# Optimization experiments

Measured on AMD Instinct MI355X. Metric: run time of the kernel, lower is better.

The kernel has to match this reference:

```python
import jax, jax.numpy as jnp
import numpy as np

B, S, SR, SN = 8, 1024, 256, 1024
D1 = 768; D2 = 512; D3 = 768; MVH = 256
H = 12; HDC = 32; HDR = 32; HD = 64
MLP_DIM = 3072
LN_EPS = 1e-6

def _ln(x, w):
    mu = jnp.mean(x, axis=-1, keepdims=True)
    var = jnp.var(x, axis=-1, keepdims=True)
    return (x - mu) * jax.lax.rsqrt(var + LN_EPS) * w

def _rope(x, freqs):
    # x: [B,H,S,dr]; freqs: [S, dr//2] (learned RoPE param)
    emb = jnp.concatenate([freqs, freqs], axis=-1)
    cos = jnp.cos(emb); sin = jnp.sin(emb)
    d = x.shape[-1] // 2
    rot = jnp.concatenate([-x[..., d:], x[..., :d]], axis=-1)
    return x * cos + rot * sin

def _rope_freqs(seq, dim, theta=10.0):
    inv_freq = 1.0 / theta ** (np.arange(0, dim, 2, dtype=np.float32) / dim)
    t = np.arange(seq, dtype=np.float32)
    return jnp.asarray(np.outer(t, inv_freq))

def setup_inputs():
    key = jax.random.key(0)
    ks = iter(jax.random.split(key, 48))
    n = lambda shape, s=0.02: jax.random.normal(next(ks), shape, jnp.float32) * s
    return dict(
        input_q=jax.random.normal(next(ks), (B, S, D1), jnp.float32),
        ln_q_w=jnp.ones((D1,), jnp.float32), ln_kv_w=jnp.ones((D1,), jnp.float32),
        Wt_mq=n((SR, S)), Wt_vq=n((SR, S)), Wt_mkv=n((SR, S)), Wt_vkv=n((SR, S)),
        mq_w1=n((D2, D1)), mq_w2=n((MVH, D2)),
        vq_w1=n((D2, D1)), vq_w2=n((MVH, D2)),
        mkv_w1=n((D2, D1)), mkv_w2=n((MVH, D2)),
        vkv_w1=n((D2, D1)), vkv_w2=n((MVH, D2)),
        dirty_zq=n((1, SR, MVH), 1.0), dirty_zkv=n((1, SR, MVH), 1.0),
        e2de=jnp.array([1.0], jnp.float32),
        Wt_qzu=n((SN, SR)), Wt_kzu=n((SN, SR)), Wt_vzu=n((SN, SR)),
        Wt_qr=n((SN, SR)), Wt_kr=n((SN, S)),
        qz_up=n((D2, MVH)), kz_up=n((D2, MVH)), vz_up=n((D2, MVH)),
        q_w=n((H * HDC, D2)), k_w=n((H * HDC, D2)), v_w=n((D3, D2)),
        qr_w=n((H * HDR, MVH)), kr_w=n((H * HDR, D1)),
        rope_q_freqs=_rope_freqs(SN, HDR), rope_k_freqs=_rope_freqs(SN, HDR),
        out_w=n((D3, D3)), ln2_w=jnp.ones((D3,), jnp.float32),
        mlp_w1=n((MLP_DIM, D3)), mlp_w2=n((D3, MLP_DIM)),
        eps_zq=jax.random.normal(next(ks), (B, SR, MVH), jnp.float32),
        eps_zkv=jax.random.normal(next(ks), (B, SR, MVH), jnp.float32),
    )

def reference(input_q, ln_q_w, ln_kv_w, Wt_mq, Wt_vq, Wt_mkv, Wt_vkv, mq_w1, mq_w2, vq_w1, vq_w2, mkv_w1, mkv_w2, vkv_w1, vkv_w2, dirty_zq, dirty_zkv, e2de, Wt_qzu, Wt_kzu, Wt_vzu, Wt_qr, Wt_kr, qz_up, kz_up, vz_up, q_w, k_w, v_w, qr_w, kr_w, rope_q_freqs, rope_k_freqs, out_w, ln2_w, mlp_w1, mlp_w2, eps_zq, eps_zkv):
    lin = lambda x, w: x @ w.T                       # torch Linear: W is [out, in]
    tlin = lambda x, w: jnp.einsum('bsd,rs->brd', x, w)  # Linear along seq axis
    xq = _ln(input_q, ln_q_w)
    xkv = _ln(input_q, ln_kv_w)  # input_kv = input_q (self-attention)
    # latent VAE mean/var: seq compress S->SR then feature D1->D2->MVH
    mean_zq = lin(lin(tlin(xq, Wt_mq), mq_w1), mq_w2)
    var_zq = lin(lin(tlin(xq, Wt_vq), vq_w1), vq_w2)
    mean_zkv = lin(lin(tlin(xkv, Wt_mkv), mkv_w1), mkv_w2)
    var_zkv = lin(lin(tlin(xkv, Wt_vkv), vkv_w1), vkv_w2)
    zq = mean_zq + (e2de * eps_zq + (1.0 - e2de) * dirty_zq) * jnp.exp(0.5 * var_zq)
    zkv = mean_zkv + (e2de * eps_zkv + (1.0 - e2de) * dirty_zkv) * jnp.exp(0.5 * var_zkv)
    # upsample seq SR->SN and features MVH->D2
    qz = lin(tlin(zq, Wt_qzu), qz_up)
    kz = lin(tlin(zkv, Wt_kzu), kz_up)
    vz = lin(tlin(zkv, Wt_vzu), vz_up)
    qr = lin(tlin(zq, Wt_qr), qr_w)        # [B,SN,H*HDR]
    kr = lin(tlin(input_q, Wt_kr), kr_w)   # [B,SN,H*HDR]
    qz = lin(qz, q_w); kz = lin(kz, k_w); vz = lin(vz, v_w)
    heads = lambda t, d: t.reshape(B, SN, H, d).transpose(0, 2, 1, 3)
    q = jnp.concatenate([heads(qz, HDC), _rope(heads(qr, HDR), rope_q_freqs)], axis=-1)
    k = jnp.concatenate([heads(kz, HDC), _rope(heads(kr, HDR), rope_k_freqs)], axis=-1)
    v = heads(vz, HD)
    scores = jnp.einsum('bhqd,bhkd->bhqk', q, k) / jnp.sqrt(jnp.float32(HD))
    o = jnp.einsum('bhqk,bhkd->bhqd', jax.nn.softmax(scores, axis=-1), v)
    o = o.transpose(0, 2, 1, 3).reshape(B, SN, D3)
    x = lin(o, out_w) + input_q
    y = _ln(x, ln2_w)
    y = lin(jax.nn.gelu(lin(y, mlp_w1), approximate=False), mlp_w2)
    return x + y
```

## Files before the change

kernel.cpp:

```cpp
#include <hip/hip_runtime.h>
#include <math.h>

#define B_   8
#define S_   1024
#define SR_  256
#define SN_  1024
#define D1_  768
#define D2_  512
#define D3_  768
#define MVH_ 256
#define H_   12
#define HD_  64
#define MLP_ 3072

typedef __attribute__((ext_vector_type(8))) short bf16x8;
typedef __attribute__((ext_vector_type(4))) float f32x4;

__device__ inline ushort f2bf(float f) {
  uint u = __float_as_uint(f);
  uint r = (u + 0x7fffu + ((u >> 16) & 1u)) >> 16;
  return (ushort)r;
}
__device__ inline float b2f(ushort u) { return __uint_as_float(((uint)u) << 16); }

__device__ inline void gload16(const void* g, void* l) {
  __builtin_amdgcn_global_load_lds(
      (const __attribute__((address_space(1))) void*)g,
      (__attribute__((address_space(3))) void*)l, 16, 0, 0);
}

__device__ inline int xcd_swz(int lin, int n) {
  int xcd = lin & 7, idx = lin >> 3;
  int q = n >> 3, r = n & 7;
  return (xcd < r ? xcd * (q + 1) : r * (q + 1) + (xcd - r) * q) + idx;
}

__global__ __launch_bounds__(256) void ln_dual_b(const float* __restrict__ x,
    const float* __restrict__ w1, const float* __restrict__ w2,
    ushort* __restrict__ o1, ushort* __restrict__ o2, int D) {
  int row = blockIdx.x;
  const float* xr = x + (size_t)row * D;
  int tid = threadIdx.x;
  float s = 0.f, ss = 0.f;
  for (int i = tid; i < D; i += 256) { float v = xr[i]; s += v; ss += v * v; }
  __shared__ float rs[256];
  __shared__ float rq[256];
  rs[tid] = s; rq[tid] = ss;
  __syncthreads();
  for (int off = 128; off > 0; off >>= 1) {
    if (tid < off) { rs[tid] += rs[tid + off]; rq[tid] += rq[tid + off]; }
    __syncthreads();
  }
  float mu  = rs[0] / (float)D;
  float var = rq[0] / (float)D - mu * mu;
  float inv = rsqrtf(var + 1e-6f);
  for (int i = tid; i < D; i += 256) {
    float v = (xr[i] - mu) * inv;
    o1[(size_t)row * D + i] = f2bf(v * w1[i]);
    o2[(size_t)row * D + i] = f2bf(v * w2[i]);
  }
}

__global__ __launch_bounds__(256) void ln_b(const float* __restrict__ x,
    const float* __restrict__ w, ushort* __restrict__ o, int D) {
  int row = blockIdx.x;
  const float* xr = x + (size_t)row * D;
  int tid = threadIdx.x;
  float s = 0.f, ss = 0.f;
  for (int i = tid; i < D; i += 256) { float v = xr[i]; s += v; ss += v * v; }
  __shared__ float rs[256];
  __shared__ float rq[256];
  rs[tid] = s; rq[tid] = ss;
  __syncthreads();
  for (int off = 128; off > 0; off >>= 1) {
    if (tid < off) { rs[tid] += rs[tid + off]; rq[tid] += rq[tid + off]; }
    __syncthreads();
  }
  float mu  = rs[0] / (float)D;
  float var = rq[0] / (float)D - mu * mu;
  float inv = rsqrtf(var + 1e-6f);
  for (int i = tid; i < D; i += 256) {
    float v = (xr[i] - mu) * inv;
    o[(size_t)row * D + i] = f2bf(v * w[i]);
  }
}

__global__ __launch_bounds__(256) void trans_f2b(const float* __restrict__ in,
    ushort* __restrict__ out, int R, int C, long strideEl) {
  __shared__ float tile[32][33];
  int bb = blockIdx.z;
  const float* ib = in + (size_t)bb * strideEl;
  ushort* ob = out + (size_t)bb * strideEl;
  int c0 = blockIdx.x << 5, r0 = blockIdx.y << 5;
  int tx = threadIdx.x & 31, ty = threadIdx.x >> 5;
#pragma unroll
  for (int i = 0; i < 4; ++i)
    tile[ty + 8 * i][tx] = ib[(size_t)(r0 + ty + 8 * i) * C + c0 + tx];
  __syncthreads();
#pragma unroll
  for (int i = 0; i < 4; ++i)
    ob[(size_t)(c0 + ty + 8 * i) * R + r0 + tx] = f2bf(tile[tx][ty + 8 * i]);
}

__global__ __launch_bounds__(256) void trans_b2b(const ushort* __restrict__ in,
    ushort* __restrict__ out, int R, int C, long strideEl) {
  __shared__ ushort tile[32][33];
  int bb = blockIdx.z;
  const ushort* ib = in + (size_t)bb * strideEl;
  ushort* ob = out + (size_t)bb * strideEl;
  int c0 = blockIdx.x << 5, r0 = blockIdx.y << 5;
  int tx = threadIdx.x & 31, ty = threadIdx.x >> 5;
#pragma unroll
  for (int i = 0; i < 4; ++i)
    tile[ty + 8 * i][tx] = ib[(size_t)(r0 + ty + 8 * i) * C + c0 + tx];
  __syncthreads();
#pragma unroll
  for (int i = 0; i < 4; ++i)
    ob[(size_t)(c0 + ty + 8 * i) * R + r0 + tx] = tile[tx][ty + 8 * i];
}

struct ConvTab {
  const float* src[28];
  int off[28];
  int cum[29];
};
__global__ __launch_bounds__(256) void multi_f2b(ConvTab t, ushort* __restrict__ wb,
                                                 int total4) {
  int i = blockIdx.x * 256 + threadIdx.x;
  if (i >= total4) return;
  int ti = 0;
  while (t.cum[ti + 1] <= i) ++ti;
  int j = i - t.cum[ti];
  float4 v = ((const float4*)t.src[ti])[j];
  ushort4 o;
  o.x = f2bf(v.x); o.y = f2bf(v.y); o.z = f2bf(v.z); o.w = f2bf(v.w);
  ((ushort4*)(wb + t.off[ti]))[j] = o;
}

__global__ __launch_bounds__(256) void rope_tab(const float* __restrict__ fq,
    const float* __restrict__ fk, float* __restrict__ ctq, float* __restrict__ stq,
    float* __restrict__ ctk, float* __restrict__ stk, int n) {
  int i = blockIdx.x * 256 + threadIdx.x;
  if (i >= n) return;
  float a = fq[i]; ctq[i] = cosf(a); stq[i] = sinf(a);
  float c = fk[i]; ctk[i] = cosf(c); stk[i] = sinf(c);
}

template <int EPI>
__global__ __launch_bounds__(256) void gemm_bf16(const ushort* __restrict__ A, long sA,
    const ushort* __restrict__ Bm, long sB, const float* __restrict__ R,
    void* __restrict__ Cout, long sC, int M, int N, int K) {
  int gx = gridDim.x, gy = gridDim.y;
  int nwg = gx * gy * gridDim.z;
  int lin = ((int)blockIdx.z * gy + (int)blockIdx.y) * gx + (int)blockIdx.x;
  lin = xcd_swz(lin, nwg);
  int bx = lin % gx, tt = lin / gx;
  int by = tt % gy, bb = tt / gy;
  const ushort* Ab = A + (size_t)bb * sA;
  const ushort* Bb = Bm + (size_t)bb * sB;
  __shared__ ushort As[128 * 32];
  __shared__ ushort Bs[128 * 32];
  int tid = threadIdx.x;
  int lane = tid & 63, wid = tid >> 6;
  int m0 = by << 7, n0 = bx << 7;
  int wm = (wid >> 1) << 6, wn = (wid & 1) << 6;
  f32x4 acc[4][4];
#pragma unroll
  for (int i = 0; i < 4; ++i)
#pragma unroll
    for (int j = 0; j < 4; ++j) acc[i][j] = (f32x4){0.f, 0.f, 0.f, 0.f};
  char* asb = (char*)As;
  char* bsb = (char*)Bs;
  int srow = lane >> 2;
  int skb  = (lane & 3) << 4;
  for (int k0 = 0; k0 < K; k0 += 32) {
    __syncthreads();
#pragma unroll
    for (int i = 0; i < 2; ++i) {
      int rr = wid * 32 + i * 16;
      gload16((const char*)Ab + ((size_t)(m0 + rr + srow) * K + k0) * 2 + skb,
              asb + rr * 64);
      gload16((const char*)Bb + ((size_t)(n0 + rr + srow) * K + k0) * 2 + skb,
              bsb + rr * 64);
    }
    __syncthreads();
    bf16x8 af[4], bf[4];
#pragma unroll
    for (int m = 0; m < 4; ++m)
      af[m] = *(bf16x8*)&As[(wm + m * 16 + (lane & 15)) * 32 + ((lane >> 4) << 3)];
#pragma unroll
    for (int n = 0; n < 4; ++n)
      bf[n] = *(bf16x8*)&Bs[(wn + n * 16 + (lane & 15)) * 32 + ((lane >> 4) << 3)];
#pragma unroll
    for (int m = 0; m < 4; ++m)
#pragma unroll
      for (int n = 0; n < 4; ++n)
        acc[m][n] = __builtin_amdgcn_mfma_f32_16x16x32_bf16(af[m], bf[n], acc[m][n], 0, 0, 0);
  }
  int cr = (lane >> 4) << 2, cc = lane & 15;
#pragma unroll
  for (int m = 0; m < 4; ++m)
#pragma unroll
    for (int n = 0; n < 4; ++n) {
#pragma unroll
      for (int r = 0; r < 4; ++r) {
        int row = m0 + wm + m * 16 + cr + r;
        int col = n0 + wn + n * 16 + cc;
        float v = acc[m][n][r];
        if (EPI == 0) {
          ((ushort*)Cout)[(size_t)bb * sC + (size_t)row * N + col] = f2bf(v);
        } else if (EPI == 1) {
          ((float*)Cout)[(size_t)row * N + col] = v + R[(size_t)row * N + col];
        } else {
          float y = 0.7978845608f * (v + 0.044715f * v * v * v);
          float sg = 1.0f / (1.0f + __expf(-2.0f * y));
          ((ushort*)Cout)[(size_t)row * N + col] = f2bf(v * sg);
        }
      }
    }
}

struct GrpTab {
  const ushort* A[32];
  const ushort* Bm[32];
  ushort* C[32];
};
__global__ __launch_bounds__(256) void gemm_grp(GrpTab t, int M, int N, int K) {
  int gx = gridDim.x, gy = gridDim.y;
  int nwg = gx * gy * gridDim.z;
  int lin = ((int)blockIdx.z * gy + (int)blockIdx.y) * gx + (int)blockIdx.x;
  lin = xcd_swz(lin, nwg);
  int bx = lin % gx, tt = lin / gx;
  int by = tt % gy, zz = tt / gy;
  const ushort* Ab = t.A[zz];
  const ushort* Bb = t.Bm[zz];
  ushort* Cb = t.C[zz];
  __shared__ ushort As[128 * 32];
  __shared__ ushort Bs[128 * 32];
  int tid = threadIdx.x;
  int lane = tid & 63, wid = tid >> 6;
  int m0 = by << 7, n0 = bx << 7;
  int wm = (wid >> 1) << 6, wn = (wid & 1) << 6;
  f32x4 acc[4][4];
#pragma unroll
  for (int i = 0; i < 4; ++i)
#pragma unroll
    for (int j = 0; j < 4; ++j) acc[i][j] = (f32x4){0.f, 0.f, 0.f, 0.f};
  char* asb = (char*)As;
  char* bsb = (char*)Bs;
  int srow = lane >> 2;
  int skb  = (lane & 3) << 4;
  for (int k0 = 0; k0 < K; k0 += 32) {
    __syncthreads();
#pragma unroll
    for (int i = 0; i < 2; ++i) {
      int rr = wid * 32 + i * 16;
      gload16((const char*)Ab + ((size_t)(m0 + rr + srow) * K + k0) * 2 + skb,
              asb + rr * 64);
      gload16((const char*)Bb + ((size_t)(n0 + rr + srow) * K + k0) * 2 + skb,
              bsb + rr * 64);
    }
    __syncthreads();
    bf16x8 af[4], bf[4];
#pragma unroll
    for (int m = 0; m < 4; ++m)
      af[m] = *(bf16x8*)&As[(wm + m * 16 + (lane & 15)) * 32 + ((lane >> 4) << 3)];
#pragma unroll
    for (int n = 0; n < 4; ++n)
      bf[n] = *(bf16x8*)&Bs[(wn + n * 16 + (lane & 15)) * 32 + ((lane >> 4) << 3)];
#pragma unroll
    for (int m = 0; m < 4; ++m)
#pragma unroll
      for (int n = 0; n < 4; ++n)
        acc[m][n] = __builtin_amdgcn_mfma_f32_16x16x32_bf16(af[m], bf[n], acc[m][n], 0, 0, 0);
  }
  int cr = (lane >> 4) << 2, cc = lane & 15;
#pragma unroll
  for (int m = 0; m < 4; ++m)
#pragma unroll
    for (int n = 0; n < 4; ++n) {
#pragma unroll
      for (int r = 0; r < 4; ++r) {
        int row = m0 + wm + m * 16 + cr + r;
        int col = n0 + wn + n * 16 + cc;
        Cb[(size_t)row * N + col] = f2bf(acc[m][n][r]);
      }
    }
}

__global__ __launch_bounds__(256) void z_combine_b(const ushort* __restrict__ mean,
    const ushort* __restrict__ var, const float* __restrict__ eps,
    const float* __restrict__ dirty, const float* __restrict__ e2de_p,
    ushort* __restrict__ zout, int total, int perBatch) {
  int i = blockIdx.x * 256 + threadIdx.x;
  if (i >= total) return;
  float e = e2de_p[0];
  float v = b2f(mean[i]) +
            (e * eps[i] + (1.0f - e) * dirty[i % perBatch]) * expf(0.5f * b2f(var[i]));
  zout[i] = f2bf(v);
}

__global__ __launch_bounds__(256) void pack_qk_b8(const ushort* __restrict__ zf,
    const ushort* __restrict__ rf, const float* __restrict__ ct,
    const float* __restrict__ st, ushort* __restrict__ out, float scale) {
  int i8 = blockIdx.x * 256 + threadIdx.x;
  int i = i8 << 3;
  int d0 = i & 63;
  int s = (i >> 6) & (S_ - 1);
  int bh = i >> 16;
  int b = bh / H_, h = bh % H_;
  short res[8];
  if (d0 < 32) {
    bf16x8 v = *(const bf16x8*)(zf + ((size_t)(b * S_ + s)) * (H_ * 32) + h * 32 + d0);
#pragma unroll
    for (int j = 0; j < 8; ++j) res[j] = (short)f2bf(b2f((ushort)v[j]) * scale);
  } else {
    const ushort* xr = rf + ((size_t)(b * S_ + s)) * (H_ * 32) + h * 32;
    int dr0 = d0 - 32;
    if (dr0 < 16) {
      bf16x8 xa = *(const bf16x8*)(xr + dr0);
      bf16x8 xb2 = *(const bf16x8*)(xr + dr0 + 16);
#pragma unroll
      for (int j = 0; j < 8; ++j) {
        float c = ct[s * 16 + dr0 + j], sn = st[s * 16 + dr0 + j];
        res[j] = (short)f2bf((b2f((ushort)xa[j]) * c - b2f((ushort)xb2[j]) * sn) * scale);
      }
    } else {
      bf16x8 xa = *(const bf16x8*)(xr + dr0);
      bf16x8 xb2 = *(const bf16x8*)(xr + dr0 - 16);
#pragma unroll
      for (int j = 0; j < 8; ++j) {
        float c = ct[s * 16 + dr0 - 16 + j], sn = st[s * 16 + dr0 - 16 + j];
        res[j] = (short)f2bf((b2f((ushort)xa[j]) * c + b2f((ushort)xb2[j]) * sn) * scale);
      }
    }
  }
  *(bf16x8*)(out + i) = *(bf16x8*)res;
}

__global__ __launch_bounds__(256) void pack_v_b8(const ushort* __restrict__ vzf,
    ushort* __restrict__ out) {
  int i8 = blockIdx.x * 256 + threadIdx.x;
  int i = i8 << 3;
  int d0 = i & 63;
  int s = (i >> 6) & (S_ - 1);
  int bh = i >> 16;
  int b = bh / H_, h = bh % H_;
  bf16x8 v = *(const bf16x8*)(vzf + ((size_t)(b * S_ + s)) * D3_ + h * 64 + d0);
  *(bf16x8*)(out + i) = v;
}

__global__ __launch_bounds__(256) void attn_mfma(const ushort* __restrict__ Q,
    const ushort* __restrict__ K, const ushort* __restrict__ V,
    ushort* __restrict__ O) {
  __shared__ ushort lds[16384];
  char* qc = (char*)lds;
  char* kc = (char*)lds + 8192;
  char* vc = (char*)lds + 16384;
  char* pc = (char*)lds + 24576;
  int tid = threadIdx.x, lane = tid & 63, wid = tid >> 6;
  int nwg = gridDim.x * gridDim.y;
  int lin = (int)blockIdx.y * gridDim.x + (int)blockIdx.x;
  lin = xcd_swz(lin, nwg);
  int qt = lin % gridDim.x;
  int bh = lin / gridDim.x;
  int q0 = qt << 6;
  int b = bh / H_, h = bh % H_;
  const ushort* Qb = Q + ((size_t)bh * S_ + q0) * HD_;
  const ushort* Kb = K + (size_t)bh * S_ * HD_;
  const ushort* Vb = V + (size_t)bh * S_ * HD_;
  {
    int r = tid >> 2, c0 = (tid & 3) * 32;
    const char* src = (const char*)Qb + r * 128;
    uint4 v0 = *(const uint4*)(src + c0);
    uint4 v1 = *(const uint4*)(src + c0 + 16);
    int sw = (r & 7) << 4;
    *(uint4*)(qc + r * 128 + (c0 ^ sw)) = v0;
    *(uint4*)(qc + r * 128 + ((c0 + 16) ^ sw)) = v1;
  }
  __syncthreads();
  bf16x8 aq[2];
  {
    int r = wid * 16 + (lane & 15);
    int sw = (r & 7) << 4;
#pragma unroll
    for (int kk = 0; kk < 2; ++kk) {
      int c2 = kk * 64 + ((lane >> 4) << 4);
      aq[kk] = *(bf16x8*)(qc + r * 128 + (c2 ^ sw));
    }
  }
  f32x4 o_[4];
  float m_[4], l_[4];
#pragma unroll
  for (int i = 0; i < 4; ++i) { o_[i] = (f32x4){0.f,0.f,0.f,0.f}; m_[i] = -1e30f; l_[i] = 0.f; }

  for (int kt = 0; kt < S_ / 64; ++kt) {
    __syncthreads();
    {
      int r = tid >> 2, c0 = (tid & 3) * 32;
      const char* src = (const char*)(Kb + (size_t)(kt * 64 + r) * HD_);
      uint4 v0 = *(const uint4*)(src + c0);
      uint4 v1 = *(const uint4*)(src + c0 + 16);
      int sw = (r & 7) << 4;
      *(uint4*)(kc + r * 128 + (c0 ^ sw)) = v0;
      *(uint4*)(kc + r * 128 + ((c0 + 16) ^ sw)) = v1;
    }
    {
      int kp = tid & 31, g = tid >> 5, d0 = g * 8;
      const ushort* s0 = Vb + (size_t)(kt * 64 + 2 * kp) * HD_ + d0;
      bf16x8 va = *(const bf16x8*)s0;
      bf16x8 vb2 = *(const bf16x8*)(s0 + HD_);
#pragma unroll
      for (int j = 0; j < 8; ++j) {
        int d = d0 + j;
        uint val = (uint)(ushort)va[j] | ((uint)(ushort)vb2[j] << 16);
        *(uint*)(vc + d * 128 + ((kp * 4) ^ ((d & 7) << 4))) = val;
      }
    }
    __syncthreads();
    f32x4 sacc[4];
#pragma unroll
    for (int ksub = 0; ksub < 4; ++ksub) {
      sacc[ksub] = (f32x4){0.f,0.f,0.f,0.f};
#pragma unroll
      for (int kk = 0; kk < 2; ++kk) {
        int r = ksub * 16 + (lane & 15);
        int c2 = kk * 64 + ((lane >> 4) << 4);
        bf16x8 bk = *(bf16x8*)(kc + r * 128 + (c2 ^ ((r & 7) << 4)));
        sacc[ksub] = __builtin_amdgcn_mfma_f32_16x16x32_bf16(aq[kk], bk, sacc[ksub], 0, 0, 0);
      }
    }
    float p[4][4];
#pragma unroll
    for (int rr = 0; rr < 4; ++rr) {
      float cm = fmaxf(fmaxf(sacc[0][rr], sacc[1][rr]), fmaxf(sacc[2][rr], sacc[3][rr]));
      cm = fmaxf(cm, __shfl_xor(cm, 1));
      cm = fmaxf(cm, __shfl_xor(cm, 2));
      cm = fmaxf(cm, __shfl_xor(cm, 4));
      cm = fmaxf(cm, __shfl_xor(cm, 8));
      float mn = fmaxf(m_[rr], cm);
      float al = __expf(m_[rr] - mn);
      float ps = 0.f;
#pragma unroll
      for (int ksub = 0; ksub < 4; ++ksub) {
        float pv = __expf(sacc[ksub][rr] - mn);
        p[ksub][rr] = pv;
        ps += pv;
      }
      ps += __shfl_xor(ps, 1);
      ps += __shfl_xor(ps, 2);
      ps += __shfl_xor(ps, 4);
      ps += __shfl_xor(ps, 8);
      l_[rr] = l_[rr] * al + ps;
      m_[rr] = mn;
#pragma unroll
      for (int ds = 0; ds < 4; ++ds) o_[ds][rr] *= al;
    }
#pragma unroll
    for (int ksub = 0; ksub < 4; ++ksub)
#pragma unroll
      for (int rr = 0; rr < 4; ++rr) {
        int r = wid * 16 + ((lane >> 4) << 2) + rr;
        int cb = (ksub * 16 + (lane & 15)) * 2;
        *(ushort*)(pc + r * 128 + (cb ^ ((r & 7) << 4))) = f2bf(p[ksub][rr]);
      }
#pragma unroll
    for (int kk2 = 0; kk2 < 2; ++kk2) {
      int rA = wid * 16 + (lane & 15);
      int c2 = kk2 * 64 + ((lane >> 4) << 4);
      bf16x8 ap = *(bf16x8*)(pc + rA * 128 + (c2 ^ ((rA & 7) << 4)));
#pragma unroll
      for (int ds = 0; ds < 4; ++ds) {
        int rB = ds * 16 + (lane & 15);
        bf16x8 bv = *(bf16x8*)(vc + rB * 128 + (c2 ^ ((rB & 7) << 4)));
        o_[ds] = __builtin_amdgcn_mfma_f32_16x16x32_bf16(ap, bv, o_[ds], 0, 0, 0);
      }
    }
  }
#pragma unroll
  for (int rr = 0; rr < 4; ++rr) {
    float inv = 1.f / l_[rr];
    int q = q0 + wid * 16 + ((lane >> 4) << 2) + rr;
#pragma unroll
    for (int ds = 0; ds < 4; ++ds) {
      int d = ds * 16 + (lane & 15);
      O[((size_t)(b * S_ + q)) * D3_ + h * HD_ + d] = f2bf(o_[ds][rr] * inv);
    }
  }
}

extern "C" void kernel_launch(void* const* d_in, const int* in_sizes, int n_in,
                              void* d_out, int out_size, void* d_ws, size_t ws_size,
                              hipStream_t stream) {
  const float* input_q = (const float*)d_in[0];
  const float* ln_q_w  = (const float*)d_in[1];
  const float* ln_kv_w = (const float*)d_in[2];
  const float* dirty_zq  = (const float*)d_in[15];
  const float* dirty_zkv = (const float*)d_in[16];
  const float* e2de    = (const float*)d_in[17];
  const float* rope_q_f = (const float*)d_in[31];
  const float* rope_k_f = (const float*)d_in[32];
  const float* ln2_w   = (const float*)d_in[34];
  const float* eps_zq  = (const float*)d_in[37];
  const float* eps_zkv = (const float*)d_in[38];

  ushort* wsu = (ushort*)d_ws;
  ushort* wb    = wsu;
  ushort* xq_b  = wsu + 12124160;
  ushort* xkv_b = wsu + 18415616;
  ushort* xqT   = wsu + 37289984;
  ushort* xkvT  = wsu + 43581440;
  ushort* inT   = wsu + 49872896;
  ushort* t1q   = wsu + 12124160;
  ushort* t1kv  = wsu + 15269888;
  ushort* t2b   = wsu + 24707072;
  ushort* mv    = wsu + 28901376;
  ushort* zqb   = wsu + 30998528;
  ushort* zkvb  = wsu + 31522816;
  ushort* zqT   = wsu + 32047104;
  ushort* zkvT  = wsu + 32571392;
  ushort* up    = wsu + 12124160;
  ushort* vzf   = wsu + 20512768;
  ushort* mid   = wsu + 56164352;
  ushort* tkr   = wsu + 37289984;
  ushort* qzf   = wsu + 68747264;
  ushort* kzf   = wsu + 71892992;
  ushort* qrf   = wsu + 75038720;
  ushort* krf   = wsu + 78184448;
  float*  ctq   = (float*)(wsu + 81330176);
  float*  stq   = ctq + 16384;
  float*  ctk   = ctq + 32768;
  float*  stk   = ctq + 49152;
  ushort* qp    = wsu + 12124160;
  ushort* kp    = wsu + 43581440;
  ushort* vp    = wsu + 49872896;
  ushort* ofb   = wsu + 56164352;
  float*  xb    = (float*)(wsu + 12124160);
  ushort* ylb   = wsu + 37289984;
  ushort* hm    = wsu + 43581440;

  const int W_mq = 0,       W_mkv = 524288;
  const int Wq1 = 1048576,  Wv1 = 1441792,  Wk1 = 1835008,  Wkv1 = 2228224;
  const int Wq2 = 2621440,  Wv2 = 2752512,  Wk2 = 2883584,  Wkv2 = 3014656;
  const int W_qzu = 3145728, W_kzu = 3407872, W_vzu = 3670016, W_qr = 3932160;
  const int W_kr = 4194304, W_qzup = 5242880, W_kzup = 5373952, W_vzup = 5505024;
  const int W_qw = 5636096, W_kw = 5832704,  W_vw = 6029312,  W_qrw = 6422528;
  const int W_krw = 6520832, W_ow = 6815744, W_m1 = 7405568,  W_m2 = 9764864;

  ln_dual_b<<<B_ * S_, 256, 0, stream>>>(input_q, ln_q_w, ln_kv_w, xq_b, xkv_b, D1_);

  {
    dim3 g(D1_ / 32, S_ / 32, B_);
    trans_b2b<<<g, 256, 0, stream>>>(xq_b, xqT, S_, D1_, (long)S_ * D1_);
    trans_b2b<<<g, 256, 0, stream>>>(xkv_b, xkvT, S_, D1_, (long)S_ * D1_);
    trans_f2b<<<g, 256, 0, stream>>>(input_q, inT, S_, D1_, (long)S_ * D1_);
  }

  {
    ConvTab t;
    const int srcIdx[28] = {3,4,5,6, 7,9,11,13, 8,10,12,14, 18,19,20,21, 22,
                            23,24,25, 26,27, 28, 29, 30, 33, 35, 36};
    const int sz[28] = {262144,262144,262144,262144, 393216,393216,393216,393216,
                        131072,131072,131072,131072, 262144,262144,262144,262144,
                        1048576, 131072,131072,131072, 196608,196608, 393216,
                        98304, 294912, 589824, 2359296, 2359296};
    int off = 0, c4 = 0;
    for (int i = 0; i < 28; ++i) {
      t.src[i] = (const float*)d_in[srcIdx[i]];
      t.off[i] = off;
      t.cum[i] = c4;
      off += sz[i];
      c4 += sz[i] / 4;
    }
    t.cum[28] = c4;
    multi_f2b<<<(c4 + 255) / 256, 256, 0, stream>>>(t, wb, c4);
    rope_tab<<<64, 256, 0, stream>>>(rope_q_f, rope_k_f, ctq, stq, ctk, stk, 16384);
  }

  long sXT = (long)S_ * D1_;

  {
    GrpTab t;
    for (int c = 0; c < 2; ++c)
      for (int b = 0; b < 8; ++b) {
        int z = c * 8 + b;
        t.A[z] = wb + (c == 0 ? W_mq : W_mkv);
        t.Bm[z] = (c == 0 ? xqT : xkvT) + (size_t)b * sXT;
        t.C[z] = (c == 0 ? t1q : t1kv) + (size_t)b * 512 * 768;
      }
    dim3 g(D1_ / 128, 512 / 128, 16);
    gemm_grp<<<g, 256, 0, stream>>>(t, 512, D1_, S_);
  }
  {
    GrpTab t;
    const int wo[4] = {Wq1, Wv1, Wk1, Wkv1};
    for (int c = 0; c < 4; ++c)
      for (int b = 0; b < 8; ++b) {
        int z = c * 8 + b;
        ushort* t1 = (c < 2 ? t1q : t1kv);
        t.A[z] = t1 + (size_t)b * 512 * 768 + (size_t)(c & 1) * 256 * 768;
        t.Bm[z] = wb + wo[c];
        t.C[z] = t2b + (size_t)z * 256 * 512;
      }
    dim3 g(D2_ / 128, 256 / 128, 32);
    gemm_grp<<<g, 256, 0, stream>>>(t, 256, D2_, D1_);
  }
  {
    GrpTab t;
    const int wo[4] = {Wq2, Wv2, Wk2, Wkv2};
    for (int c = 0; c < 4; ++c)
      for (int b = 0; b < 8; ++b) {
        int z = c * 8 + b;
        t.A[z] = t2b + (size_t)z * 256 * 512;
        t.Bm[z] = wb + wo[c];
        t.C[z] = mv + (size_t)z * 256 * 256;
      }
    dim3 g(MVH_ / 128, 256 / 128, 32);
    gemm_grp<<<g, 256, 0, stream>>>(t, 256, MVH_, D2_);
  }
  z_combine_b<<<(B_ * SR_ * MVH_) / 256, 256, 0, stream>>>(mv, mv + 8 * 65536,
      eps_zq, dirty_zq, e2de, zqb, B_ * SR_ * MVH_, SR_ * MVH_);
  z_combine_b<<<(B_ * SR_ * MVH_) / 256, 256, 0, stream>>>(mv + 16 * 65536,
      mv + 24 * 65536, eps_zkv, dirty_zkv, e2de, zkvb, B_ * SR_ * MVH_, SR_ * MVH_);
  {
    dim3 g(MVH_ / 32, SR_ / 32, B_);
    trans_b2b<<<g, 256, 0, stream>>>(zqb, zqT, SR_, MVH_, (long)SR_ * MVH_);
    trans_b2b<<<g, 256, 0, stream>>>(zkvb, zkvT, SR_, MVH_, (long)SR_ * MVH_);
  }
  {
    GrpTab t;
    const int wo[4] = {W_qzu, W_kzu, W_vzu, W_qr};
    for (int c = 0; c < 4; ++c)
      for (int b = 0; b < 8; ++b) {
        int z = c * 8 + b;
        t.A[z] = wb + wo[c];
        t.Bm[z] = ((c == 0 || c == 3) ? zqT : zkvT) + (size_t)b * 65536;
        t.C[z] = up + (size_t)z * 1024 * 256;
      }
    dim3 g(MVH_ / 128, SN_ / 128, 32);
    gemm_grp<<<g, 256, 0, stream>>>(t, SN_, MVH_, SR_);
  }
  {
    GrpTab t;
    const int wo[3] = {W_qzup, W_kzup, W_vzup};
    for (int c = 0; c < 3; ++c) {
      t.A[c] = up + (size_t)c * 8 * 1024 * 256;
      t.Bm[c] = wb + wo[c];
      t.C[c] = mid + (size_t)c * 8192 * 512;
    }
    dim3 g(D2_ / 128, (B_ * SN_) / 128, 3);
    gemm_grp<<<g, 256, 0, stream>>>(t, B_ * SN_, D2_, MVH_);
  }
  {
    dim3 g(384 / 128, (B_ * SN_) / 128, 1);
    gemm_bf16<0><<<g, 256, 0, stream>>>(up + (size_t)3 * 8 * 1024 * 256, 0,
        wb + W_qrw, 0, nullptr, qrf, 0, B_ * SN_, 384, MVH_);
  }
  {
    GrpTab t;
    t.A[0] = mid;                      t.Bm[0] = wb + W_qw; t.C[0] = qzf;
    t.A[1] = mid + (size_t)8192 * 512; t.Bm[1] = wb + W_kw; t.C[1] = kzf;
    dim3 g(384 / 128, (B_ * SN_) / 128, 2);
    gemm_grp<<<g, 256, 0, stream>>>(t, B_ * SN_, 384, D2_);
  }
  {
    dim3 g(D3_ / 128, (B_ * SN_) / 128, 1);
    gemm_bf16<0><<<g, 256, 0, stream>>>(mid + (size_t)2 * 8192 * 512, 0,
        wb + W_vw, 0, nullptr, vzf, 0, B_ * SN_, D3_, D2_);
  }
  {
    dim3 g(D1_ / 128, SN_ / 128, B_);
    gemm_bf16<0><<<g, 256, 0, stream>>>(wb + W_kr, 0, inT, sXT, nullptr, tkr,
        (long)SN_ * D1_, SN_, D1_, S_);
  }
  {
    dim3 g(384 / 128, (B_ * SN_) / 128, 1);
    gemm_bf16<0><<<g, 256, 0, stream>>>(tkr, 0, wb + W_krw, 0, nullptr, krf, 0,
        B_ * SN_, 384, D1_);
  }

  int chunks = (B_ * H_ * S_ * HD_) / 8;
  pack_qk_b8<<<chunks / 256, 256, 0, stream>>>(qzf, qrf, ctq, stq, qp, 0.125f);
  pack_qk_b8<<<chunks / 256, 256, 0, stream>>>(kzf, krf, ctk, stk, kp, 1.0f);
  pack_v_b8<<<chunks / 256, 256, 0, stream>>>(vzf, vp);

  {
    dim3 g(S_ / 64, B_ * H_);
    attn_mfma<<<g, 256, 0, stream>>>(qp, kp, vp, ofb);
  }

  {
    dim3 g(D3_ / 128, (B_ * SN_) / 128);
    gemm_bf16<1><<<g, 256, 0, stream>>>(ofb, 0, wb + W_ow, 0, input_q, xb, 0,
                                        B_ * SN_, D3_, D3_);
  }
  ln_b<<<B_ * SN_, 256, 0, stream>>>(xb, ln2_w, ylb, D3_);
  {
    dim3 g(MLP_ / 128, (B_ * SN_) / 128);
    gemm_bf16<2><<<g, 256, 0, stream>>>(ylb, 0, wb + W_m1, 0, nullptr, hm, 0,
                                        B_ * SN_, MLP_, D3_);
  }
  {
    dim3 g(D3_ / 128, (B_ * SN_) / 128);
    gemm_bf16<1><<<g, 256, 0, stream>>>(hm, 0, wb + W_m2, 0, xb, (float*)d_out, 0,
                                        B_ * SN_, D3_, MLP_);
  }
}
```

Baseline: 542.9 us.

## Enlarge attention query tile to 128 rows per block, reusing K/V tiles

The attention kernel now processes 128 query rows per workgroup instead of 64, with each wave handling two 16-row sub-blocks that share each loaded K and V fragment. This halves the K/V global loads and LDS staging per query and halves the grid size. It also brackets the MFMA sections with s_setprio to favour matrix work. The cost is more registers per thread, a larger LDS footprint and fewer workgroups (768), which may lower occupancy.

```diff
diff --git a/kernel.cpp b/kernel.cpp
--- a/kernel.cpp
+++ b/kernel.cpp
@@ -353,46 +353,53 @@
 __global__ __launch_bounds__(256) void attn_mfma(const ushort* __restrict__ Q,
     const ushort* __restrict__ K, const ushort* __restrict__ V,
     ushort* __restrict__ O) {
-  __shared__ ushort lds[16384];
+  __shared__ ushort lds[24576];
   char* qc = (char*)lds;
-  char* kc = (char*)lds + 8192;
-  char* vc = (char*)lds + 16384;
-  char* pc = (char*)lds + 24576;
+  char* kc = (char*)lds + 16384;
+  char* vc = (char*)lds + 24576;
+  char* pc = (char*)lds + 32768;
   int tid = threadIdx.x, lane = tid & 63, wid = tid >> 6;
   int nwg = gridDim.x * gridDim.y;
   int lin = (int)blockIdx.y * gridDim.x + (int)blockIdx.x;
   lin = xcd_swz(lin, nwg);
   int qt = lin % gridDim.x;
   int bh = lin / gridDim.x;
-  int q0 = qt << 6;
+  int q0 = qt << 7;
   int b = bh / H_, h = bh % H_;
   const ushort* Qb = Q + ((size_t)bh * S_ + q0) * HD_;
   const ushort* Kb = K + (size_t)bh * S_ * HD_;
   const ushort* Vb = V + (size_t)bh * S_ * HD_;
   {
-    int r = tid >> 2, c0 = (tid & 3) * 32;
-    const char* src = (const char*)Qb + r * 128;
-    uint4 v0 = *(const uint4*)(src + c0);
-    uint4 v1 = *(const uint4*)(src + c0 + 16);
+    int r = tid >> 1, c0 = (tid & 1) * 64;
+    const char* src = (const char*)Qb + r * 128 + c0;
     int sw = (r & 7) << 4;
-    *(uint4*)(qc + r * 128 + (c0 ^ sw)) = v0;
-    *(uint4*)(qc + r * 128 + ((c0 + 16) ^ sw)) = v1;
+#pragma unroll
+    for (int j = 0; j < 4; ++j) {
+      uint4 v = *(const uint4*)(src + j * 16);
+      *(uint4*)(qc + r * 128 + ((c0 + j * 16) ^ sw)) = v;
+    }
   }
   __syncthreads();
-  bf16x8 aq[2];
-  {
-    int r = wid * 16 + (lane & 15);
+  bf16x8 aq[2][2];
+#pragma unroll
+  for (int rb = 0; rb < 2; ++rb) {
+    int r = wid * 32 + rb * 16 + (lane & 15);
     int sw = (r & 7) << 4;
 #pragma unroll
     for (int kk = 0; kk < 2; ++kk) {
       int c2 = kk * 64 + ((lane >> 4) << 4);
-      aq[kk] = *(bf16x8*)(qc + r * 128 + (c2 ^ sw));
-    }
-  }
-  f32x4 o_[4];
-  float m_[4], l_[4];
-#pragma unroll
-  for (int i = 0; i < 4; ++i) { o_[i] = (f32x4){0.f,0.f,0.f,0.f}; m_[i] = -1e30f; l_[i] = 0.f; }
+      aq[rb][kk] = *(bf16x8*)(qc + r * 128 + (c2 ^ sw));
+    }
+  }
+  f32x4 o_[2][4];
+  float m_[2][4], l_[2][4];
+#pragma unroll
+  for (int rb = 0; rb < 2; ++rb)
+#pragma unroll
+    for (int i = 0; i < 4; ++i) {
+      o_[rb][i] = (f32x4){0.f, 0.f, 0.f, 0.f};
+      m_[rb][i] = -1e30f; l_[rb][i] = 0.f;
+    }
 
   for (int kt = 0; kt < S_ / 64; ++kt) {
     __syncthreads();
@@ -418,75 +425,91 @@
       }
     }
     __syncthreads();
-    f32x4 sacc[4];
+    f32x4 sacc[2][4];
+    __builtin_amdgcn_s_setprio(1);
 #pragma unroll
     for (int ksub = 0; ksub < 4; ++ksub) {
-      sacc[ksub] = (f32x4){0.f,0.f,0.f,0.f};
+      sacc[0][ksub] = (f32x4){0.f, 0.f, 0.f, 0.f};
+      sacc[1][ksub] = (f32x4){0.f, 0.f, 0.f, 0.f};
 #pragma unroll
       for (int kk = 0; kk < 2; ++kk) {
         int r = ksub * 16 + (lane & 15);
         int c2 = kk * 64 + ((lane >> 4) << 4);
         bf16x8 bk = *(bf16x8*)(kc + r * 128 + (c2 ^ ((r & 7) << 4)));
-        sacc[ksub] = __builtin_amdgcn_mfma_f32_16x16x32_bf16(aq[kk], bk, sacc[ksub], 0, 0, 0);
-      }
-    }
-    float p[4][4];
-#pragma unroll
-    for (int rr = 0; rr < 4; ++rr) {
-      float cm = fmaxf(fmaxf(sacc[0][rr], sacc[1][rr]), fmaxf(sacc[2][rr], sacc[3][rr]));
-      cm = fmaxf(cm, __shfl_xor(cm, 1));
-      cm = fmaxf(cm, __shfl_xor(cm, 2));
-      cm = fmaxf(cm, __shfl_xor(cm, 4));
-      cm = fmaxf(cm, __shfl_xor(cm, 8));
-      float mn = fmaxf(m_[rr], cm);
-      float al = __expf(m_[rr] - mn);
-      float ps = 0.f;
-#pragma unroll
-      for (int ksub = 0; ksub < 4; ++ksub) {
-        float pv = __expf(sacc[ksub][rr] - mn);
-        p[ksub][rr] = pv;
-        ps += pv;
-      }
-      ps += __shfl_xor(ps, 1);
-      ps += __shfl_xor(ps, 2);
-      ps += __shfl_xor(ps, 4);
-      ps += __shfl_xor(ps, 8);
-      l_[rr] = l_[rr] * al + ps;
-      m_[rr] = mn;
-#pragma unroll
-      for (int ds = 0; ds < 4; ++ds) o_[ds][rr] *= al;
-    }
-#pragma unroll
-    for (int ksub = 0; ksub < 4; ++ksub)
+        sacc[0][ksub] = __builtin_amdgcn_mfma_f32_16x16x32_bf16(aq[0][kk], bk, sacc[0][ksub], 0, 0, 0);
+        sacc[1][ksub] = __builtin_amdgcn_mfma_f32_16x16x32_bf16(aq[1][kk], bk, sacc[1][ksub], 0, 0, 0);
+      }
+    }
+    __builtin_amdgcn_s_setprio(0);
+    float p[2][4][4];
+#pragma unroll
+    for (int rb = 0; rb < 2; ++rb)
 #pragma unroll
       for (int rr = 0; rr < 4; ++rr) {
-        int r = wid * 16 + ((lane >> 4) << 2) + rr;
-        int cb = (ksub * 16 + (lane & 15)) * 2;
-        *(ushort*)(pc + r * 128 + (cb ^ ((r & 7) << 4))) = f2bf(p[ksub][rr]);
-      }
+        float cm = fmaxf(fmaxf(sacc[rb][0][rr], sacc[rb][1][rr]),
+                         fmaxf(sacc[rb][2][rr], sacc[rb][3][rr]));
+        cm = fmaxf(cm, __shfl_xor(cm, 1));
+        cm = fmaxf(cm, __shfl_xor(cm, 2));
+        cm = fmaxf(cm, __shfl_xor(cm, 4));
+        cm = fmaxf(cm, __shfl_xor(cm, 8));
+        float mn = fmaxf(m_[rb][rr], cm);
+        float al = __expf(m_[rb][rr] - mn);
+        float ps = 0.f;
+#pragma unroll
+        for (int ksub = 0; ksub < 4; ++ksub) {
+          float pv = __expf(sacc[rb][ksub][rr] - mn);
+          p[rb][ksub][rr] = pv;
+          ps += pv;
+        }
+        ps += __shfl_xor(ps, 1);
+        ps += __shfl_xor(ps, 2);
+        ps += __shfl_xor(ps, 4);
+        ps += __shfl_xor(ps, 8);
+        l_[rb][rr] = l_[rb][rr] * al + ps;
+        m_[rb][rr] = mn;
+#pragma unroll
+        for (int ds = 0; ds < 4; ++ds) o_[rb][ds][rr] *= al;
+      }
+#pragma unroll
+    for (int rb = 0; rb < 2; ++rb)
+#pragma unroll
+      for (int ksub = 0; ksub < 4; ++ksub)
+#pragma unroll
+        for (int rr = 0; rr < 4; ++rr) {
+          int r = wid * 32 + rb * 16 + ((lane >> 4) << 2) + rr;
+          int cb = (ksub * 16 + (lane & 15)) * 2;
+          *(ushort*)(pc + r * 128 + (cb ^ ((r & 7) << 4))) = f2bf(p[rb][ksub][rr]);
+        }
+    __builtin_amdgcn_s_setprio(1);
 #pragma unroll
     for (int kk2 = 0; kk2 < 2; ++kk2) {
-      int rA = wid * 16 + (lane & 15);
       int c2 = kk2 * 64 + ((lane >> 4) << 4);
-      bf16x8 ap = *(bf16x8*)(pc + rA * 128 + (c2 ^ ((rA & 7) << 4)));
+      int rA0 = wid * 32 + (lane & 15);
+      int rA1 = rA0 + 16;
+      bf16x8 ap0 = *(bf16x8*)(pc + rA0 * 128 + (c2 ^ ((rA0 & 7) << 4)));
+      bf16x8 ap1 = *(bf16x8*)(pc + rA1 * 128 + (c2 ^ ((rA1 & 7) << 4)));
 #pragma unroll
       for (int ds = 0; ds < 4; ++ds) {
         int rB = ds * 16 + (lane & 15);
         bf16x8 bv = *(bf16x8*)(vc + rB * 128 + (c2 ^ ((rB & 7) << 4)));
-        o_[ds] = __builtin_amdgcn_mfma_f32_16x16x32_bf16(ap, bv, o_[ds], 0, 0, 0);
-      }
-    }
-  }
-#pragma unroll
-  for (int rr = 0; rr < 4; ++rr) {
-    float inv = 1.f / l_[rr];
-    int q = q0 + wid * 16 + ((lane >> 4) << 2) + rr;
-#pragma unroll
-    for (int ds = 0; ds < 4; ++ds) {
-      int d = ds * 16 + (lane & 15);
-      O[((size_t)(b * S_ + q)) * D3_ + h * HD_ + d] = f2bf(o_[ds][rr] * inv);
-    }
-  }
+        o_[0][ds] = __builtin_amdgcn_mfma_f32_16x16x32_bf16(ap0, bv, o_[0][ds], 0, 0, 0);
+        o_[1][ds] = __builtin_amdgcn_mfma_f32_16x16x32_bf16(ap1, bv, o_[1][ds], 0, 0, 0);
+      }
+    }
+    __builtin_amdgcn_s_setprio(0);
+  }
+#pragma unroll
+  for (int rb = 0; rb < 2; ++rb)
+#pragma unroll
+    for (int rr = 0; rr < 4; ++rr) {
+      float inv = 1.f / l_[rb][rr];
+      int q = q0 + wid * 32 + rb * 16 + ((lane >> 4) << 2) + rr;
+#pragma unroll
+      for (int ds = 0; ds < 4; ++ds) {
+        int d = ds * 16 + (lane & 15);
+        O[((size_t)(b * S_ + q)) * D3_ + h * HD_ + d] = f2bf(o_[rb][ds][rr] * inv);
+      }
+    }
 }
 
 extern "C" void kernel_launch(void* const* d_in, const int* in_sizes, int n_in,
@@ -685,7 +708,7 @@
   pack_v_b8<<<chunks / 256, 256, 0, stream>>>(vzf, vp);
 
   {
-    dim3 g(S_ / 64, B_ * H_);
+    dim3 g(S_ / 128, B_ * H_);
     attn_mfma<<<g, 256, 0, stream>>>(qp, kp, vp, ofb);
   }
 
```

After: 547.8 us. About the same (+0.9%).
